# Kernel optimization log

Measured on AMD Instinct MI355X. Metric: run time of the kernel, lower is better.

The kernel has to match this reference:

```python
import jax, jax.numpy as jnp
import numpy as np


def setup_inputs() -> dict:
    key = jax.random.key(0)
    k1, k2, k3, k4 = jax.random.split(key, 4)
    N, E, d_i, d_o = 4096, 32768, 128, 128
    x = jax.random.normal(k1, (N, d_i), dtype=jnp.float32)
    src = jax.random.uniform(k2, (N, E), dtype=jnp.float32)
    tgt = jax.random.uniform(k3, (N, E), dtype=jnp.float32)
    # Linear(2*d_i, d_o): weight [d_o, 2*d_i] (xavier-like scale), bias zeros
    f_w = jax.random.normal(k4, (d_o, 2 * d_i), dtype=jnp.float32) * (1.0 / np.sqrt(2 * d_i))
    f_b = jnp.zeros((d_o,), dtype=jnp.float32)
    return {"x": x, "src": src, "tgt": tgt, "f_w": f_w, "f_b": f_b}


def reference(x, src, tgt, f_w, f_b):
    # gather node features to edges via dense incidence matmuls
    hsrc = src.T @ x                      # [E, d_i]
    htgt = tgt.T @ x                      # [E, d_i]
    h = jnp.concatenate([hsrc, htgt], axis=1)  # [E, 2*d_i]
    y = jax.nn.relu(h @ f_w.T + f_b)      # [E, d_o]
    return tgt @ y                        # scatter back to nodes: [N, d_o]
```

## Files before the change

### kernel.cpp

```cpp
#include <hip/hip_runtime.h>

typedef __attribute__((ext_vector_type(8))) short short8v;
typedef __attribute__((ext_vector_type(4))) float float4v;
typedef __attribute__((ext_vector_type(2))) unsigned int u32x2;
typedef __attribute__((ext_vector_type(4))) unsigned int u32x4;
typedef unsigned short u16;
typedef unsigned int u32;
typedef const __attribute__((address_space(1))) void* gas1;
typedef __attribute__((address_space(3))) void* las3;

#define NN 4096
#define EE 32768
#define DI 128
#define DO 128

__device__ __forceinline__ u16 f2bf(float f) {
    u32 u = __builtin_bit_cast(u32, f);
    u32 r = u + 0x7fffu + ((u >> 16) & 1u);
    return (u16)(r >> 16);
}
__device__ __forceinline__ u32 pack2bf(float lo, float hi) {
    return (u32)f2bf(lo) | ((u32)f2bf(hi) << 16);
}
__device__ __forceinline__ void gload16(const void* g, void* l) {
    __builtin_amdgcn_global_load_lds((gas1)g, (las3)l, 16, 0, 0);
}
__device__ __forceinline__ u32 cvtpk(float lo, float hi) {
    u32 r;
    asm("v_cvt_pk_bf16_f32 %0, %1, %2" : "=v"(r) : "v"(lo), "v"(hi));
    return r;
}

template<int R, int C>
__device__ __forceinline__ void stage_f32_bf16(char* lds, const float* src, int ld) {
    constexpr int CH = C / 8;
    constexpr int ITER = (R * CH) / 256;
#pragma unroll
    for (int it = 0; it < ITER; ++it) {
        int c = it * 256 + (int)threadIdx.x;
        int row = c / CH, col8 = c % CH;
        const float* p = src + (size_t)row * ld + col8 * 8;
        float4v v0 = *(const float4v*)p;
        float4v v1 = *(const float4v*)(p + 4);
        u32x4 w;
        w[0] = pack2bf(v0[0], v0[1]);
        w[1] = pack2bf(v0[2], v0[3]);
        w[2] = pack2bf(v1[0], v1[1]);
        w[3] = pack2bf(v1[2], v1[3]);
        int kb = col8 * 16;
        *(u32x4*)(lds + row * (C * 2) + (kb ^ ((row & 7) << 4))) = w;
    }
}
template<int ROWB>
__device__ __forceinline__ short8v ldfrag(const char* base, int row16, int kk) {
    int l = (int)threadIdx.x & 63;
    int row = row16 + (l & 15);
    int kb = kk * 64 + ((l >> 4) << 4);
    return *(const short8v*)(base + row * ROWB + (kb ^ ((row & 7) << 4)));
}

__global__ __launch_bounds__(256) void k1_ab(const float* __restrict__ x,
                                             const float* __restrict__ fw,
                                             u16* __restrict__ ATB) {
    __shared__ __align__(16) char lds[64 * 1024];
    char* aL = lds;
    char* bL = lds + 32 * 1024;
    int mb = (int)blockIdx.x >> 5, nb = (int)blockIdx.x & 31;
    stage_f32_bf16<128, 128>(aL, fw + mb * 128, 2 * DI);
    stage_f32_bf16<128, 128>(bL, x + (size_t)nb * 128 * DI, DI);
    __syncthreads();
    int w = (int)threadIdx.x >> 6, l = (int)threadIdx.x & 63;
    int wr = w >> 1, wc = w & 1;
    float4v acc[4][4] = {};
#pragma unroll
    for (int kk = 0; kk < 4; ++kk) {
        short8v af[4], bf[4];
#pragma unroll
        for (int m = 0; m < 4; ++m) af[m] = ldfrag<256>(aL, wr * 64 + m * 16, kk);
#pragma unroll
        for (int n2 = 0; n2 < 4; ++n2) bf[n2] = ldfrag<256>(bL, wc * 64 + n2 * 16, kk);
#pragma unroll
        for (int m = 0; m < 4; ++m)
#pragma unroll
            for (int n2 = 0; n2 < 4; ++n2)
                acc[m][n2] = __builtin_amdgcn_mfma_f32_16x16x32_bf16(af[m], bf[n2], acc[m][n2], 0, 0, 0);
    }
#pragma unroll
    for (int m = 0; m < 4; ++m)
#pragma unroll
        for (int n2 = 0; n2 < 4; ++n2)
#pragma unroll
            for (int r = 0; r < 4; ++r) {
                int mo = mb * 128 + wr * 64 + m * 16 + ((l >> 4) << 2) + r;
                int n  = nb * 128 + wc * 64 + n2 * 16 + (l & 15);
                ATB[(size_t)mo * NN + n] = f2bf(acc[m][n2][r]);
            }
}

__global__ __launch_bounds__(256, 3) void k2_y(const float* __restrict__ src,
                                               const float* __restrict__ tgt,
                                               const u16* __restrict__ ATB,
                                               const float* __restrict__ fb,
                                               u16* __restrict__ YT) {
    __shared__ __align__(16) char lds[48 * 1024];
    const int eb = (int)blockIdx.x * 64;
    const int t = (int)threadIdx.x, w = t >> 6, l = t & 63;
    const int eq = t & 15, nq = t >> 4;

    auto loadT = [&](int ks, float4v& r0, float4v& r1, float4v& r2, float4v& r3) {
        const float* M = (ks >= 64 ? tgt : src);
        const int n0 = (ks & 63) * 64;
        const float* p = M + (size_t)(n0 + nq * 4) * EE + eb + eq * 4;
        r0 = *(const float4v*)p;
        r1 = *(const float4v*)(p + EE);
        r2 = *(const float4v*)(p + 2 * EE);
        r3 = *(const float4v*)(p + 3 * EE);
    };
    auto gloadA = [&](int ks, int p) {
        const int mat = ks >> 6, n0 = (ks & 63) * 64;
        const u16* AB = ATB + (size_t)mat * 128 * NN + n0;
#pragma unroll
        for (int q = 0; q < 4; ++q) {
            const int s = w * 4 + q;
            const int r = s * 8 + (l >> 3);
            const u16* ga = AB + (size_t)r * NN + (((l & 7) ^ (r & 7)) << 3);
            gload16(ga, lds + p * 16384 + s * 1024);
        }
    };
    auto writeT = [&](int p, float4v& r0, float4v& r1, float4v& r2, float4v& r3) {
        char* buf = lds + 32768 + p * 8192;
#pragma unroll
        for (int j = 0; j < 4; ++j) {
            int e = eq * 4 + j;
            u32x2 w2;
            w2[0] = cvtpk(r0[j], r1[j]);
            w2[1] = cvtpk(r2[j], r3[j]);
            *(u32x2*)(buf + e * 128 + ((nq * 8) ^ ((e & 7) << 4))) = w2;
        }
    };

    float4v acc[2][4] = {};
    auto step = [&](int ks, float4v& c0, float4v& c1, float4v& c2, float4v& c3,
                    float4v& x0, float4v& x1, float4v& x2, float4v& x3) {
        const int nx2 = ks + 2 < 128 ? ks + 2 : 127;
        const int nx1 = ks + 1 < 128 ? ks + 1 : 127;
        loadT(nx2, c0, c1, c2, c3);
        gloadA(nx1, (ks + 1) & 1);
        asm volatile("s_waitcnt vmcnt(8)" ::: "memory");
        __builtin_amdgcn_sched_barrier(0);
        const char* bufA = lds + (ks & 1) * 16384;
        const char* bufB = lds + 32768 + (ks & 1) * 8192;
        short8v af[2][2], bfr[2][4];
#pragma unroll
        for (int kk = 0; kk < 2; ++kk) {
#pragma unroll
            for (int m = 0; m < 2; ++m)
                af[kk][m] = ldfrag<128>(bufA, w * 32 + m * 16, kk);
#pragma unroll
            for (int n2 = 0; n2 < 4; ++n2)
                bfr[kk][n2] = ldfrag<128>(bufB, n2 * 16, kk);
        }
#pragma unroll
        for (int kk = 0; kk < 2; ++kk)
#pragma unroll
            for (int m = 0; m < 2; ++m)
#pragma unroll
                for (int n2 = 0; n2 < 4; ++n2)
                    acc[m][n2] = __builtin_amdgcn_mfma_f32_16x16x32_bf16(
                        af[kk][m], bfr[kk][n2], acc[m][n2], 0, 0, 0);
        writeT((ks + 1) & 1, x0, x1, x2, x3);
        asm volatile("s_waitcnt lgkmcnt(0)" ::: "memory");
        __builtin_amdgcn_sched_barrier(0);
        __builtin_amdgcn_s_barrier();
    };

    float4v a0, a1, a2, a3, b0, b1, b2, b3;
    loadT(0, a0, a1, a2, a3);
    asm volatile("s_waitcnt vmcnt(0)" ::: "memory");
    writeT(0, a0, a1, a2, a3);
    loadT(1, b0, b1, b2, b3);
    gloadA(0, 0);
    __syncthreads();

    for (int ks = 0; ks < 128; ks += 2) {
        step(ks,     a0, a1, a2, a3,  b0, b1, b2, b3);
        step(ks + 1, b0, b1, b2, b3,  a0, a1, a2, a3);
    }
#pragma unroll
    for (int m = 0; m < 2; ++m)
#pragma unroll
        for (int n2 = 0; n2 < 4; ++n2)
#pragma unroll
            for (int r = 0; r < 4; ++r) {
                const int o = w * 32 + m * 16 + ((l >> 4) << 2) + r;
                const int e = eb + n2 * 16 + (l & 15);
                float v = acc[m][n2][r] + fb[o];
                v = v > 0.f ? v : 0.f;
                YT[(size_t)o * EE + e] = f2bf(v);
            }
}

__global__ __launch_bounds__(256, 3) void k3_part(const float* __restrict__ tgt,
                                                  const u16* __restrict__ YT,
                                                  float* __restrict__ part) {
    __shared__ __align__(16) char lds[48 * 1024];
    const int bid = (int)blockIdx.x;
    const int mb = bid & 63, kc = bid >> 6;
    const int e0 = kc * 2048;
    const int t = (int)threadIdx.x, w = t >> 6, l = t & 63;
    const int wr = w >> 1, wc = w & 1;
    const int trow = t >> 2, te0 = (t & 3) * 16;

    float4v v0, v1, v2, v3;
    auto loadT = [&](int es) {
        const float* p = tgt + (size_t)(mb * 64 + trow) * EE + e0 + es * 64 + te0;
        v0 = *(const float4v*)p;
        v1 = *(const float4v*)(p + 4);
        v2 = *(const float4v*)(p + 8);
        v3 = *(const float4v*)(p + 12);
    };
    auto gloadY = [&](int es, int p) {
        const int ec = e0 + es * 64;
#pragma unroll
        for (int q = 0; q < 4; ++q) {
            const int s = w * 4 + q;
            const int r = s * 8 + (l >> 3);
            const u16* gy = YT + (size_t)r * EE + ec + (((l & 7) ^ (r & 7)) << 3);
            gload16(gy, lds + 16384 + p * 16384 + s * 1024);
        }
    };
    auto writeT = [&](int p) {
        char* buf = lds + p * 8192;
        u32x4 wA, wB;
        wA[0] = cvtpk(v0[0], v0[1]); wA[1] = cvtpk(v0[2], v0[3]);
        wA[2] = cvtpk(v1[0], v1[1]); wA[3] = cvtpk(v1[2], v1[3]);
        wB[0] = cvtpk(v2[0], v2[1]); wB[1] = cvtpk(v2[2], v2[3]);
        wB[2] = cvtpk(v3[0], v3[1]); wB[3] = cvtpk(v3[2], v3[3]);
        *(u32x4*)(buf + trow * 128 + ((te0 * 2) ^ ((trow & 7) << 4))) = wA;
        *(u32x4*)(buf + trow * 128 + ((te0 * 2 + 16) ^ ((trow & 7) << 4))) = wB;
    };

    loadT(0);
    gloadY(0, 0);
    writeT(0);
    __syncthreads();

    float4v acc[2][4] = {};
    for (int es = 0; es < 32; ++es) {
        const int nx = es < 31 ? es + 1 : 31;
        loadT(nx);
        gloadY(nx, (es + 1) & 1);
        asm volatile("s_waitcnt vmcnt(8)" ::: "memory");
        __builtin_amdgcn_sched_barrier(0);
        __builtin_amdgcn_s_barrier();
        const char* bufT = lds + (es & 1) * 8192;
        const char* bufY = lds + 16384 + (es & 1) * 16384;
        short8v af[2][2], bfr[2][4];
#pragma unroll
        for (int kk = 0; kk < 2; ++kk) {
#pragma unroll
            for (int m = 0; m < 2; ++m)
                af[kk][m] = ldfrag<128>(bufT, wr * 32 + m * 16, kk);
#pragma unroll
            for (int n2 = 0; n2 < 4; ++n2)
                bfr[kk][n2] = ldfrag<128>(bufY, wc * 64 + n2 * 16, kk);
        }
#pragma unroll
        for (int kk = 0; kk < 2; ++kk)
#pragma unroll
            for (int m = 0; m < 2; ++m)
#pragma unroll
                for (int n2 = 0; n2 < 4; ++n2)
                    acc[m][n2] = __builtin_amdgcn_mfma_f32_16x16x32_bf16(
                        af[kk][m], bfr[kk][n2], acc[m][n2], 0, 0, 0);
        asm volatile("s_waitcnt vmcnt(4)" ::: "memory");
        __builtin_amdgcn_sched_barrier(0);
        writeT((es + 1) & 1);
        asm volatile("s_waitcnt lgkmcnt(0)" ::: "memory");
        __builtin_amdgcn_sched_barrier(0);
        __builtin_amdgcn_s_barrier();
    }
#pragma unroll
    for (int m = 0; m < 2; ++m)
#pragma unroll
        for (int n2 = 0; n2 < 4; ++n2)
#pragma unroll
            for (int r = 0; r < 4; ++r) {
                const int n = mb * 64 + wr * 32 + m * 16 + ((l >> 4) << 2) + r;
                const int o = wc * 64 + n2 * 16 + (l & 15);
                part[((size_t)kc * NN + n) * DO + o] = acc[m][n2][r];
            }
}

__global__ __launch_bounds__(256) void k4_red(const float* __restrict__ part,
                                              float* __restrict__ out) {
    size_t i = ((size_t)blockIdx.x * 256 + threadIdx.x) * 4;
    float4v s = {0.f, 0.f, 0.f, 0.f};
#pragma unroll
    for (int kc = 0; kc < 16; ++kc)
        s += *(const float4v*)(part + (size_t)kc * NN * DO + i);
    *(float4v*)(out + i) = s;
}

extern "C" void kernel_launch(void* const* d_in, const int* in_sizes, int n_in,
                              void* d_out, int out_size, void* d_ws, size_t ws_size,
                              hipStream_t stream) {
    const float* x   = (const float*)d_in[0];
    const float* src = (const float*)d_in[1];
    const float* tgt = (const float*)d_in[2];
    const float* fw  = (const float*)d_in[3];
    const float* fb  = (const float*)d_in[4];
    float* out = (float*)d_out;

    char* ws = (char*)d_ws;
    u16*   ATB  = (u16*)ws;
    u16*   YT   = (u16*)(ws + (size_t)2 * 1024 * 1024);
    float* PART = (float*)(ws + (size_t)16 * 1024 * 1024);

    k1_ab  <<<64,   256, 0, stream>>>(x, fw, ATB);
    k2_y   <<<512,  256, 0, stream>>>(src, tgt, ATB, fb, YT);
    k3_part<<<1024, 256, 0, stream>>>(tgt, YT, PART);
    k4_red <<<512,  256, 0, stream>>>(PART, out);
}
```

Baseline: 374.3 us.

## Load k2 A-operand fragments directly into registers instead of staging through LDS

In the k2_y kernel, the bf16 A operand (ATB) was copied global-to-LDS with async 16-byte loads and then read back as MFMA fragments. It is now loaded straight from global memory into per-wave registers in fragment layout, double-buffered across steps in registers. This cuts LDS use from 48 KB to 16 KB, which may allow more resident blocks, and removes LDS read traffic for A. In exchange it adds register pressure and uncoalesced, row-strided global reads of ATB. The explicit vmcnt wait was dropped, so the compiler now has to insert the waits on the register loads.

```diff
diff --git a/kernel.cpp b/kernel.cpp
--- a/kernel.cpp
+++ b/kernel.cpp
@@ -102,12 +102,12 @@
                                                const u16* __restrict__ ATB,
                                                const float* __restrict__ fb,
                                                u16* __restrict__ YT) {
-    __shared__ __align__(16) char lds[48 * 1024];
+    __shared__ __align__(16) char lds[16 * 1024];
     const int eb = (int)blockIdx.x * 64;
     const int t = (int)threadIdx.x, w = t >> 6, l = t & 63;
     const int eq = t & 15, nq = t >> 4;
 
-    auto loadT = [&](int ks, float4v& r0, float4v& r1, float4v& r2, float4v& r3) {
+    auto loadM = [&](int ks, float4v& r0, float4v& r1, float4v& r2, float4v& r3) {
         const float* M = (ks >= 64 ? tgt : src);
         const int n0 = (ks & 63) * 64;
         const float* p = M + (size_t)(n0 + nq * 4) * EE + eb + eq * 4;
@@ -116,19 +116,17 @@
         r2 = *(const float4v*)(p + 2 * EE);
         r3 = *(const float4v*)(p + 3 * EE);
     };
-    auto gloadA = [&](int ks, int p) {
+    auto loadA = [&](int ks, short8v& A00, short8v& A01, short8v& A10, short8v& A11) {
         const int mat = ks >> 6, n0 = (ks & 63) * 64;
-        const u16* AB = ATB + (size_t)mat * 128 * NN + n0;
-#pragma unroll
-        for (int q = 0; q < 4; ++q) {
-            const int s = w * 4 + q;
-            const int r = s * 8 + (l >> 3);
-            const u16* ga = AB + (size_t)r * NN + (((l & 7) ^ (r & 7)) << 3);
-            gload16(ga, lds + p * 16384 + s * 1024);
-        }
+        const u16* base = ATB + (size_t)(mat * 128 + w * 32 + (l & 15)) * NN
+                          + n0 + ((l >> 4) << 3);
+        A00 = *(const short8v*)(base);
+        A01 = *(const short8v*)(base + 32);
+        A10 = *(const short8v*)(base + (size_t)16 * NN);
+        A11 = *(const short8v*)(base + (size_t)16 * NN + 32);
     };
     auto writeT = [&](int p, float4v& r0, float4v& r1, float4v& r2, float4v& r3) {
-        char* buf = lds + 32768 + p * 8192;
+        char* buf = lds + p * 8192;
 #pragma unroll
         for (int j = 0; j < 4; ++j) {
             int e = eq * 4 + j;
@@ -140,51 +138,49 @@
     };
 
     float4v acc[2][4] = {};
-    auto step = [&](int ks, float4v& c0, float4v& c1, float4v& c2, float4v& c3,
-                    float4v& x0, float4v& x1, float4v& x2, float4v& x3) {
+    auto step = [&](int ks,
+                    short8v& c00, short8v& c01, short8v& c10, short8v& c11,
+                    short8v& x00, short8v& x01, short8v& x10, short8v& x11,
+                    float4v& m0, float4v& m1, float4v& m2, float4v& m3,
+                    float4v& y0, float4v& y1, float4v& y2, float4v& y3) {
         const int nx2 = ks + 2 < 128 ? ks + 2 : 127;
         const int nx1 = ks + 1 < 128 ? ks + 1 : 127;
-        loadT(nx2, c0, c1, c2, c3);
-        gloadA(nx1, (ks + 1) & 1);
-        asm volatile("s_waitcnt vmcnt(8)" ::: "memory");
-        __builtin_amdgcn_sched_barrier(0);
-        const char* bufA = lds + (ks & 1) * 16384;
-        const char* bufB = lds + 32768 + (ks & 1) * 8192;
-        short8v af[2][2], bfr[2][4];
-#pragma unroll
-        for (int kk = 0; kk < 2; ++kk) {
-#pragma unroll
-            for (int m = 0; m < 2; ++m)
-                af[kk][m] = ldfrag<128>(bufA, w * 32 + m * 16, kk);
+        loadM(nx2, m0, m1, m2, m3);
+        loadA(nx1, x00, x01, x10, x11);
+        const char* bufB = lds + (ks & 1) * 8192;
+        short8v bfr[2][4];
+#pragma unroll
+        for (int kk = 0; kk < 2; ++kk)
 #pragma unroll
             for (int n2 = 0; n2 < 4; ++n2)
                 bfr[kk][n2] = ldfrag<128>(bufB, n2 * 16, kk);
+#pragma unroll
+        for (int n2 = 0; n2 < 4; ++n2) {
+            acc[0][n2] = __builtin_amdgcn_mfma_f32_16x16x32_bf16(c00, bfr[0][n2], acc[0][n2], 0, 0, 0);
+            acc[1][n2] = __builtin_amdgcn_mfma_f32_16x16x32_bf16(c10, bfr[0][n2], acc[1][n2], 0, 0, 0);
+            acc[0][n2] = __builtin_amdgcn_mfma_f32_16x16x32_bf16(c01, bfr[1][n2], acc[0][n2], 0, 0, 0);
+            acc[1][n2] = __builtin_amdgcn_mfma_f32_16x16x32_bf16(c11, bfr[1][n2], acc[1][n2], 0, 0, 0);
         }
-#pragma unroll
-        for (int kk = 0; kk < 2; ++kk)
-#pragma unroll
-            for (int m = 0; m < 2; ++m)
-#pragma unroll
-                for (int n2 = 0; n2 < 4; ++n2)
-                    acc[m][n2] = __builtin_amdgcn_mfma_f32_16x16x32_bf16(
-                        af[kk][m], bfr[kk][n2], acc[m][n2], 0, 0, 0);
-        writeT((ks + 1) & 1, x0, x1, x2, x3);
+        writeT((ks + 1) & 1, y0, y1, y2, y3);
         asm volatile("s_waitcnt lgkmcnt(0)" ::: "memory");
         __builtin_amdgcn_sched_barrier(0);
         __builtin_amdgcn_s_barrier();
     };
 
-    float4v a0, a1, a2, a3, b0, b1, b2, b3;
-    loadT(0, a0, a1, a2, a3);
+    float4v aM0, aM1, aM2, aM3, bM0, bM1, bM2, bM3;
+    short8v aA00, aA01, aA10, aA11, bA00, bA01, bA10, bA11;
+    loadM(0, aM0, aM1, aM2, aM3);
     asm volatile("s_waitcnt vmcnt(0)" ::: "memory");
-    writeT(0, a0, a1, a2, a3);
-    loadT(1, b0, b1, b2, b3);
-    gloadA(0, 0);
+    writeT(0, aM0, aM1, aM2, aM3);
+    loadA(0, aA00, aA01, aA10, aA11);
+    loadM(1, bM0, bM1, bM2, bM3);
     __syncthreads();
 
     for (int ks = 0; ks < 128; ks += 2) {
-        step(ks,     a0, a1, a2, a3,  b0, b1, b2, b3);
-        step(ks + 1, b0, b1, b2, b3,  a0, a1, a2, a3);
+        step(ks,     aA00, aA01, aA10, aA11,  bA00, bA01, bA10, bA11,
+                     aM0, aM1, aM2, aM3,      bM0, bM1, bM2, bM3);
+        step(ks + 1, bA00, bA01, bA10, bA11,  aA00, aA01, aA10, aA11,
+                     bM0, bM1, bM2, bM3,      aM0, aM1, aM2, aM3);
     }
 #pragma unroll
     for (int m = 0; m < 2; ++m)
```

Result: faster. 367.0 us (-2.0%).
